# Kernel optimization log

Hardware: AMD Instinct MI355X
Metric: run time of the kernel (lower is better)

## Reference

```python
import jax, jax.numpy as jnp
import numpy as np

WIN = 7
DIM = 384
HEADS = 12
HEAD_DIM = DIM // HEADS


def relative_position_index(win):
    ch = np.arange(win)
    cw = np.arange(win)
    coords = np.stack(np.meshgrid(ch, cw, indexing='ij'))  # [2,w,w]
    cf = coords.reshape(2, -1)
    rel = cf[:, :, None] - cf[:, None, :]  # [2,ww,ww]
    rel = rel.transpose(1, 2, 0)
    rel[:, :, 0] += win - 1
    rel[:, :, 1] += win - 1
    rel[:, :, 0] *= 2 * win - 1
    return jnp.array(rel.sum(-1), dtype=jnp.int32)  # [ww,ww]


def setup_inputs() -> dict:
    key = jax.random.key(0)
    ks = jax.random.split(key, 9)
    B, S = 1024, WIN * WIN
    M = 16  # windows per image
    s = 1.0 / np.sqrt(DIM)
    return {
        'hidden_states': jax.random.normal(ks[0], (B, S, DIM), jnp.float32),
        'attention_mask': jax.random.normal(ks[1], (M, S, S), jnp.float32),
        'Wq': jax.random.normal(ks[2], (DIM, DIM), jnp.float32) * s,
        'bq': jnp.zeros((DIM,), jnp.float32),
        'Wk': jax.random.normal(ks[3], (DIM, DIM), jnp.float32) * s,
        'bk': jnp.zeros((DIM,), jnp.float32),
        'Wv': jax.random.normal(ks[4], (DIM, DIM), jnp.float32) * s,
        'bv': jnp.zeros((DIM,), jnp.float32),
        'rel_bias_table': jax.random.normal(ks[5], ((2 * WIN - 1) ** 2, HEADS), jnp.float32) * 0.02,
        'rel_index': relative_position_index(WIN),
    }


def reference(hidden_states, attention_mask, Wq, bq, Wk, bk, Wv, bv, rel_bias_table, rel_index):
    B, S, _ = hidden_states.shape
    q = (hidden_states @ Wq + bq).reshape(B, S, HEADS, HEAD_DIM)
    k = (hidden_states @ Wk + bk).reshape(B, S, HEADS, HEAD_DIM)
    v = (hidden_states @ Wv + bv).reshape(B, S, HEADS, HEAD_DIM)
    q = q / jnp.sqrt(jnp.float32(HEAD_DIM)).astype(q.dtype)
    attn = jnp.einsum('bqhd,bkhd->bhqk', q, k)  # [B,H,S,S]
    # relative position bias: gather + reshape + transpose -> [1,H,S,S]
    bias = rel_bias_table[rel_index.reshape(-1)].reshape(S, S, HEADS)
    attn = attn + jnp.transpose(bias, (2, 0, 1))[None]
    # shifted-window mask add: [B//M, M, H, S, S]
    Mw = attention_mask.shape[0]
    attn = attn.reshape(B // Mw, Mw, HEADS, S, S) + attention_mask[None, :, None, :, :]
    attn = attn.reshape(B, HEADS, S, S)
    attn = jax.nn.softmax(attn, axis=-1)
    out = jnp.einsum('bhqk,bkhd->bqhd', attn, v).reshape(B, S, DIM)
    return out
```

## Files before the change

### kernel.cpp

```cpp
#include <hip/hip_runtime.h>

typedef __attribute__((ext_vector_type(8))) short short8;
typedef __attribute__((ext_vector_type(4))) float f32x4;

__device__ __forceinline__ unsigned short f2bf(float f) {
  unsigned u = __builtin_bit_cast(unsigned, f);
  u += 0x7fffu + ((u >> 16) & 1u);
  return (unsigned short)(u >> 16);
}

__global__ __launch_bounds__(256) void k_prepw(const float* __restrict__ Wq, const float* __restrict__ Wk,
                                               const float* __restrict__ Wv, const float* __restrict__ bq,
                                               const float* __restrict__ bk, const float* __restrict__ bv,
                                               unsigned short* __restrict__ Wt, float* __restrict__ bvec) {
  int i = blockIdx.x * 256 + threadIdx.x;
  int n = i / 384, k = i - n * 384;
  int which = n / 384;
  int c = n - which * 384;
  const float* W = (which == 0) ? Wq : (which == 1) ? Wk : Wv;
  Wt[i] = f2bf(W[k * 384 + c]);
  if (k == 0) {
    const float* bb = (which == 0) ? bq : (which == 1) ? bk : bv;
    bvec[n] = bb[c];
  }
}

__global__ __launch_bounds__(256) void k_prept(const float* __restrict__ tab, const int* __restrict__ ridx,
                                               const float* __restrict__ am, float* __restrict__ T) {
  int i = blockIdx.x * 256 + threadIdx.x;
  int lane = i & 63;
  int rest = i >> 6;
  int ik = rest & 3, jq = (rest >> 2) & 3, wh = rest >> 4;
  int h = wh % 12, w = wh / 12;
  int lr = lane & 15, lg = lane >> 4;
  int q = jq * 16 + lr;
  f32x4 v;
  #pragma unroll
  for (int r = 0; r < 4; ++r) {
    int k = ik * 16 + lg * 4 + r;
    v[r] = (q < 49 && k < 49) ? tab[ridx[q * 49 + k] * 12 + h] + am[w * 2401 + q * 49 + k] : 0.f;
  }
  *(f32x4*)(T + (size_t)i * 4) = v;
}

__global__ __launch_bounds__(384, 3) void k_mega(const float* __restrict__ X,
                                                 const unsigned short* __restrict__ Wt,
                                                 const float* __restrict__ bvec,
                                                 const float* __restrict__ T,
                                                 float* __restrict__ out) {
  extern __shared__ unsigned short pool[];
  const int bid = blockIdx.x;
  const int w = bid >> 1, half = bid & 1;
  const int tid = threadIdx.x;
  const int lane = tid & 63, wid = tid >> 6;
  const int head = half * 6 + wid;
  const int lr = lane & 15, lg = lane >> 4;
  char* poolB = (char*)pool;

  #pragma unroll
  for (int it = 0; it < 8; ++it) {
    int c = tid + 384 * it;
    int row = c / 48, c8 = c - row * 48;
    short8 v = {0, 0, 0, 0, 0, 0, 0, 0};
    if (row < 49) {
      const float* p = X + ((size_t)(w * 49 + row)) * 384 + c8 * 8;
      f32x4 f0 = *(const f32x4*)p;
      f32x4 f1 = *(const f32x4*)(p + 4);
      v[0] = (short)f2bf(f0[0]); v[1] = (short)f2bf(f0[1]); v[2] = (short)f2bf(f0[2]); v[3] = (short)f2bf(f0[3]);
      v[4] = (short)f2bf(f1[0]); v[5] = (short)f2bf(f1[1]); v[6] = (short)f2bf(f1[2]); v[7] = (short)f2bf(f1[3]);
    }
    *(short8*)(poolB + row * 768 + ((c8 * 16) ^ ((row & 7) << 4))) = v;
  }
  __syncthreads();

  const unsigned swz = (unsigned)((lr & 7) << 4);
  unsigned hq[16], hk[16], hv[16];
  #pragma unroll
  for (int p = 0; p < 3; ++p) {
    const unsigned short* Bg = Wt + ((size_t)(p * 384 + head * 32 + lr)) * 384 + lg * 8;
    f32x4 acc[4][2] = {};
    short8 bB[4][2];
    #pragma unroll
    for (int k0 = 0; k0 < 3; ++k0) {
      bB[k0][0] = *(const short8*)(Bg + k0 * 32);
      bB[k0][1] = *(const short8*)(Bg + 16 * 384 + k0 * 32);
    }
    #pragma unroll
    for (int k = 0; k < 12; ++k) {
      if (k + 3 < 12) {
        bB[(k + 3) & 3][0] = *(const short8*)(Bg + (k + 3) * 32);
        bB[(k + 3) & 3][1] = *(const short8*)(Bg + 16 * 384 + (k + 3) * 32);
      }
      short8 aC[4];
      #pragma unroll
      for (int mi = 0; mi < 4; ++mi)
        aC[mi] = *(const short8*)(poolB + (16 * mi + lr) * 768 + (unsigned)((k * 64 + lg * 16) ^ swz));
      __builtin_amdgcn_s_setprio(1);
      #pragma unroll
      for (int mi = 0; mi < 4; ++mi)
        #pragma unroll
        for (int ni = 0; ni < 2; ++ni)
          acc[mi][ni] = __builtin_amdgcn_mfma_f32_16x16x32_bf16(aC[mi], bB[k & 3][ni], acc[mi][ni], 0, 0, 0);
      __builtin_amdgcn_s_setprio(0);
    }
    float scl = (p == 0) ? 0.17677669529663687f : 1.0f;
    unsigned* hd = (p == 0) ? hq : (p == 1) ? hk : hv;
    float b0 = bvec[p * 384 + head * 32 + lr];
    float b1 = bvec[p * 384 + head * 32 + 16 + lr];
    #pragma unroll
    for (int mi = 0; mi < 4; ++mi)
      #pragma unroll
      for (int ni = 0; ni < 2; ++ni) {
        float bb = ni ? b1 : b0;
        float v0 = (acc[mi][ni][0] + bb) * scl;
        float v1 = (acc[mi][ni][1] + bb) * scl;
        float v2 = (acc[mi][ni][2] + bb) * scl;
        float v3 = (acc[mi][ni][3] + bb) * scl;
        hd[(mi * 2 + ni) * 2 + 0] = (unsigned)f2bf(v0) | ((unsigned)f2bf(v1) << 16);
        hd[(mi * 2 + ni) * 2 + 1] = (unsigned)f2bf(v2) | ((unsigned)f2bf(v3) << 16);
      }
  }
  __syncthreads();

  unsigned short* reg = pool + wid * 6400;
  unsigned short* Qs = reg;
  unsigned short* Ks = reg + 1984;
  unsigned short* Vt = reg + 4096;
  char* Pb = (char*)reg;
  #pragma unroll
  for (int mi = 0; mi < 4; ++mi)
    #pragma unroll
    for (int ni = 0; ni < 2; ++ni) {
      int d = ni * 16 + lr;
      #pragma unroll
      for (int e = 0; e < 2; ++e) {
        int s0 = 16 * mi + 4 * lg + 2 * e;
        *(unsigned*)&Vt[d * 72 + s0] = hv[(mi * 2 + ni) * 2 + e];
      }
      #pragma unroll
      for (int r = 0; r < 4; ++r) {
        int s = 16 * mi + 4 * lg + r;
        if (s < 49) {
          unsigned short qv = (unsigned short)(hq[(mi * 2 + ni) * 2 + (r >> 1)] >> ((r & 1) * 16));
          unsigned short kv = (unsigned short)(hk[(mi * 2 + ni) * 2 + (r >> 1)] >> ((r & 1) * 16));
          Qs[s * 40 + d] = qv;
          Ks[s * 40 + d] = kv;
        }
      }
    }

  short8 qf[4], kf[4];
  #pragma unroll
  for (int t = 0; t < 4; ++t) {
    int rq = t * 16 + lr; if (rq > 48) rq = 48;
    qf[t] = *(const short8*)&Qs[rq * 40 + lg * 8];
    kf[t] = *(const short8*)&Ks[rq * 40 + lg * 8];
  }
  f32x4 sc[4][4] = {};
  #pragma unroll
  for (int ik = 0; ik < 4; ++ik)
    #pragma unroll
    for (int jq = 0; jq < 4; ++jq)
      sc[ik][jq] = __builtin_amdgcn_mfma_f32_16x16x32_bf16(kf[ik], qf[jq], sc[ik][jq], 0, 0, 0);

  const float* Tb = T + ((size_t)((w & 15) * 12 + head)) * 4096;
  #pragma unroll
  for (int jq = 0; jq < 4; ++jq) {
    #pragma unroll
    for (int ik = 0; ik < 4; ++ik) {
      f32x4 tv = *(const f32x4*)(Tb + ((jq * 4 + ik) * 64 + lane) * 4);
      #pragma unroll
      for (int r = 0; r < 4; ++r) {
        float v = sc[ik][jq][r] + tv[r];
        if (ik == 3) {
          if (r == 0) v = (lg == 0) ? v : -1e30f;
          else v = -1e30f;
        }
        sc[ik][jq][r] = v;
      }
    }
    float m = -1e30f;
    #pragma unroll
    for (int ik = 0; ik < 4; ++ik)
      #pragma unroll
      for (int r = 0; r < 4; ++r) m = fmaxf(m, sc[ik][jq][r]);
    m = fmaxf(m, __shfl_xor(m, 16));
    m = fmaxf(m, __shfl_xor(m, 32));
    float s = 0.f;
    #pragma unroll
    for (int ik = 0; ik < 4; ++ik)
      #pragma unroll
      for (int r = 0; r < 4; ++r) {
        float e = __expf(sc[ik][jq][r] - m);
        sc[ik][jq][r] = e;
        s += e;
      }
    s += __shfl_xor(s, 16);
    s += __shfl_xor(s, 32);
    float iv = 1.0f / s;
    int q = jq * 16 + lr;
    #pragma unroll
    for (int ik = 0; ik < 4; ++ik) {
      unsigned d0 = (unsigned)f2bf(sc[ik][jq][0] * iv) | ((unsigned)f2bf(sc[ik][jq][1] * iv) << 16);
      unsigned d1 = (unsigned)f2bf(sc[ik][jq][2] * iv) | ((unsigned)f2bf(sc[ik][jq][3] * iv) << 16);
      unsigned off = (unsigned)(q * 128 + ik * 32 + lg * 8) ^ ((unsigned)(lr & 7) << 4);
      *(uint2*)(Pb + off) = make_uint2(d0, d1);
    }
  }

  short8 vf[2][2];
  #pragma unroll
  for (int kk = 0; kk < 2; ++kk)
    #pragma unroll
    for (int nl = 0; nl < 2; ++nl)
      vf[kk][nl] = *(const short8*)&Vt[(nl * 16 + lr) * 72 + kk * 32 + lg * 8];
  f32x4 ao[4][2] = {};
  #pragma unroll
  for (int i = 0; i < 4; ++i) {
    short8 pf[2];
    #pragma unroll
    for (int kk = 0; kk < 2; ++kk) {
      unsigned off = (unsigned)((i * 16 + lr) * 128 + (kk * 4 + lg) * 16) ^ ((unsigned)(lr & 7) << 4);
      pf[kk] = *(const short8*)(Pb + off);
    }
    #pragma unroll
    for (int nl = 0; nl < 2; ++nl)
      #pragma unroll
      for (int kk = 0; kk < 2; ++kk)
        ao[i][nl] = __builtin_amdgcn_mfma_f32_16x16x32_bf16(pf[kk], vf[kk][nl], ao[i][nl], 0, 0, 0);
  }

  #pragma unroll
  for (int i = 0; i < 4; ++i) {
    #pragma unroll
    for (int j2 = 0; j2 < 4; ++j2) {
      int q = i * 16 + lg * 4 + j2;
      if (q < 49) {
        #pragma unroll
        for (int nl = 0; nl < 2; ++nl) {
          int d = nl * 16 + lr;
          out[((size_t)(w * 49 + q)) * 384 + head * 32 + d] = ao[i][nl][j2];
        }
      }
    }
  }
}

extern "C" void kernel_launch(void* const* d_in, const int* in_sizes, int n_in,
                              void* d_out, int out_size, void* d_ws, size_t ws_size,
                              hipStream_t stream) {
  const float* hs  = (const float*)d_in[0];
  const float* am  = (const float*)d_in[1];
  const float* Wq  = (const float*)d_in[2];
  const float* bq  = (const float*)d_in[3];
  const float* Wk  = (const float*)d_in[4];
  const float* bk  = (const float*)d_in[5];
  const float* Wv  = (const float*)d_in[6];
  const float* bv  = (const float*)d_in[7];
  const float* tab = (const float*)d_in[8];
  const int*   rix = (const int*)d_in[9];
  float* out = (float*)d_out;
  char* ws = (char*)d_ws;

  size_t o = 0;
  auto alloc = [&](size_t bytes) { size_t r = o; o = (o + bytes + 255) & ~(size_t)255; return r; };
  unsigned short* Wt   = (unsigned short*)(ws + alloc(1152ull * 384 * 2));
  float*          bvec = (float*)(ws + alloc(1152ull * 4));
  float*          Tt   = (float*)(ws + alloc(192ull * 4096 * 4));
  (void)ws_size; (void)in_sizes; (void)n_in; (void)out_size;

  hipFuncSetAttribute((const void*)k_mega, hipFuncAttributeMaxDynamicSharedMemorySize, 76800);

  k_prepw<<<1728, 256, 0, stream>>>(Wq, Wk, Wv, bq, bk, bv, Wt, bvec);
  k_prept<<<768, 256, 0, stream>>>(tab, rix, am, Tt);
  k_mega<<<2048, 384, 76800, stream>>>(hs, Wt, bvec, Tt, out);
}
```

Baseline: 318.5 us.

## Keep Q/K/P fragments in registers via transposed MFMA layouts, shrink LDS

The QKV projection now computes W^T·X^T, so the accumulator output lands directly in the fragment layout needed by 16x16x16 MFMAs for the scores and the PV product. This removes the LDS round trips for Q, K and P. Softmax normalisation is deferred to the output, which allows vectorized float4 stores. The V projection is moved after softmax, and LDS drops to 48KB, which could allow more blocks per CU. Block IDs are remapped to spread windows across XCDs. The cost is higher register pressure from holding the qfr, kfr and pfr fragments.

```diff
diff --git a/kernel.cpp b/kernel.cpp
--- a/kernel.cpp
+++ b/kernel.cpp
@@ -1,6 +1,7 @@
 #include <hip/hip_runtime.h>
 
 typedef __attribute__((ext_vector_type(8))) short short8;
+typedef __attribute__((ext_vector_type(4))) short s16x4;
 typedef __attribute__((ext_vector_type(4))) float f32x4;
 
 __device__ __forceinline__ unsigned short f2bf(float f) {
@@ -8,6 +9,16 @@
   u += 0x7fffu + ((u >> 16) & 1u);
   return (unsigned short)(u >> 16);
 }
+
+#if __has_builtin(__builtin_amdgcn_mfma_f32_16x16x16bf16_1k)
+#define MFMA16(A, B, C) __builtin_amdgcn_mfma_f32_16x16x16bf16_1k((A), (B), (C), 0, 0, 0)
+#else
+__device__ __forceinline__ f32x4 mfma16_asm(s16x4 a, s16x4 b, f32x4 c) {
+  asm volatile("v_mfma_f32_16x16x16_bf16 %0, %1, %2, %0" : "+v"(c) : "v"(a), "v"(b));
+  return c;
+}
+#define MFMA16(A, B, C) mfma16_asm((A), (B), (C))
+#endif
 
 __global__ __launch_bounds__(256) void k_prepw(const float* __restrict__ Wq, const float* __restrict__ Wk,
                                                const float* __restrict__ Wv, const float* __restrict__ bq,
@@ -49,13 +60,15 @@
                                                  const float* __restrict__ T,
                                                  float* __restrict__ out) {
   extern __shared__ unsigned short pool[];
-  const int bid = blockIdx.x;
+  int orig = blockIdx.x;
+  int bid = (orig & 7) * 256 + (orig >> 3);
   const int w = bid >> 1, half = bid & 1;
   const int tid = threadIdx.x;
   const int lane = tid & 63, wid = tid >> 6;
   const int head = half * 6 + wid;
   const int lr = lane & 15, lg = lane >> 4;
   char* poolB = (char*)pool;
+  const unsigned swz = (unsigned)((lr & 7) << 4);
 
   #pragma unroll
   for (int it = 0; it < 8; ++it) {
@@ -73,97 +86,62 @@
   }
   __syncthreads();
 
-  const unsigned swz = (unsigned)((lr & 7) << 4);
-  unsigned hq[16], hk[16], hv[16];
-  #pragma unroll
-  for (int p = 0; p < 3; ++p) {
-    const unsigned short* Bg = Wt + ((size_t)(p * 384 + head * 32 + lr)) * 384 + lg * 8;
-    f32x4 acc[4][2] = {};
-    short8 bB[4][2];
-    #pragma unroll
-    for (int k0 = 0; k0 < 3; ++k0) {
-      bB[k0][0] = *(const short8*)(Bg + k0 * 32);
-      bB[k0][1] = *(const short8*)(Bg + 16 * 384 + k0 * 32);
-    }
+  auto run_pass = [&](int p, float scl, s16x4 fr[2][4]) {
+    const unsigned short* Wg = Wt + ((size_t)(p * 384 + head * 32 + lr)) * 384 + lg * 8;
+    f32x4 acc[2][4] = {};
+    short8 wC[2], wN[2];
+    wC[0] = *(const short8*)(Wg);
+    wC[1] = *(const short8*)(Wg + 6144);
     #pragma unroll
     for (int k = 0; k < 12; ++k) {
-      if (k + 3 < 12) {
-        bB[(k + 3) & 3][0] = *(const short8*)(Bg + (k + 3) * 32);
-        bB[(k + 3) & 3][1] = *(const short8*)(Bg + 16 * 384 + (k + 3) * 32);
-      }
-      short8 aC[4];
-      #pragma unroll
-      for (int mi = 0; mi < 4; ++mi)
-        aC[mi] = *(const short8*)(poolB + (16 * mi + lr) * 768 + (unsigned)((k * 64 + lg * 16) ^ swz));
+      if (k < 11) {
+        wN[0] = *(const short8*)(Wg + (k + 1) * 32);
+        wN[1] = *(const short8*)(Wg + 6144 + (k + 1) * 32);
+      }
+      short8 xf[4];
+      #pragma unroll
+      for (int ni = 0; ni < 4; ++ni)
+        xf[ni] = *(const short8*)(poolB + (16 * ni + lr) * 768 + (unsigned)((k * 64 + lg * 16) ^ swz));
       __builtin_amdgcn_s_setprio(1);
       #pragma unroll
-      for (int mi = 0; mi < 4; ++mi)
+      for (int mi = 0; mi < 2; ++mi)
         #pragma unroll
-        for (int ni = 0; ni < 2; ++ni)
-          acc[mi][ni] = __builtin_amdgcn_mfma_f32_16x16x32_bf16(aC[mi], bB[k & 3][ni], acc[mi][ni], 0, 0, 0);
+        for (int ni = 0; ni < 4; ++ni)
+          acc[mi][ni] = __builtin_amdgcn_mfma_f32_16x16x32_bf16(wC[mi], xf[ni], acc[mi][ni], 0, 0, 0);
       __builtin_amdgcn_s_setprio(0);
-    }
-    float scl = (p == 0) ? 0.17677669529663687f : 1.0f;
-    unsigned* hd = (p == 0) ? hq : (p == 1) ? hk : hv;
-    float b0 = bvec[p * 384 + head * 32 + lr];
-    float b1 = bvec[p * 384 + head * 32 + 16 + lr];
-    #pragma unroll
-    for (int mi = 0; mi < 4; ++mi)
-      #pragma unroll
-      for (int ni = 0; ni < 2; ++ni) {
-        float bb = ni ? b1 : b0;
-        float v0 = (acc[mi][ni][0] + bb) * scl;
-        float v1 = (acc[mi][ni][1] + bb) * scl;
-        float v2 = (acc[mi][ni][2] + bb) * scl;
-        float v3 = (acc[mi][ni][3] + bb) * scl;
-        hd[(mi * 2 + ni) * 2 + 0] = (unsigned)f2bf(v0) | ((unsigned)f2bf(v1) << 16);
-        hd[(mi * 2 + ni) * 2 + 1] = (unsigned)f2bf(v2) | ((unsigned)f2bf(v3) << 16);
-      }
-  }
-  __syncthreads();
-
-  unsigned short* reg = pool + wid * 6400;
-  unsigned short* Qs = reg;
-  unsigned short* Ks = reg + 1984;
-  unsigned short* Vt = reg + 4096;
-  char* Pb = (char*)reg;
-  #pragma unroll
-  for (int mi = 0; mi < 4; ++mi)
-    #pragma unroll
-    for (int ni = 0; ni < 2; ++ni) {
-      int d = ni * 16 + lr;
-      #pragma unroll
-      for (int e = 0; e < 2; ++e) {
-        int s0 = 16 * mi + 4 * lg + 2 * e;
-        *(unsigned*)&Vt[d * 72 + s0] = hv[(mi * 2 + ni) * 2 + e];
-      }
-      #pragma unroll
-      for (int r = 0; r < 4; ++r) {
-        int s = 16 * mi + 4 * lg + r;
-        if (s < 49) {
-          unsigned short qv = (unsigned short)(hq[(mi * 2 + ni) * 2 + (r >> 1)] >> ((r & 1) * 16));
-          unsigned short kv = (unsigned short)(hk[(mi * 2 + ni) * 2 + (r >> 1)] >> ((r & 1) * 16));
-          Qs[s * 40 + d] = qv;
-          Ks[s * 40 + d] = kv;
-        }
-      }
-    }
-
-  short8 qf[4], kf[4];
-  #pragma unroll
-  for (int t = 0; t < 4; ++t) {
-    int rq = t * 16 + lr; if (rq > 48) rq = 48;
-    qf[t] = *(const short8*)&Qs[rq * 40 + lg * 8];
-    kf[t] = *(const short8*)&Ks[rq * 40 + lg * 8];
-  }
+      wC[0] = wN[0]; wC[1] = wN[1];
+    }
+    #pragma unroll
+    for (int mi = 0; mi < 2; ++mi) {
+      f32x4 bv = *(const f32x4*)(bvec + p * 384 + head * 32 + 16 * mi + 4 * lg);
+      #pragma unroll
+      for (int ni = 0; ni < 4; ++ni) {
+        s16x4 o;
+        #pragma unroll
+        for (int r = 0; r < 4; ++r) o[r] = (short)f2bf((acc[mi][ni][r] + bv[r]) * scl);
+        fr[mi][ni] = o;
+      }
+    }
+  };
+
+  s16x4 qfr[2][4], kfr[2][4];
+  run_pass(0, 0.17677669529663687f, qfr);
+  run_pass(1, 1.0f, kfr);
+
   f32x4 sc[4][4] = {};
-  #pragma unroll
-  for (int ik = 0; ik < 4; ++ik)
-    #pragma unroll
-    for (int jq = 0; jq < 4; ++jq)
-      sc[ik][jq] = __builtin_amdgcn_mfma_f32_16x16x32_bf16(kf[ik], qf[jq], sc[ik][jq], 0, 0, 0);
+  __builtin_amdgcn_s_setprio(1);
+  #pragma unroll
+  for (int dblk = 0; dblk < 2; ++dblk)
+    #pragma unroll
+    for (int ik = 0; ik < 4; ++ik)
+      #pragma unroll
+      for (int jq = 0; jq < 4; ++jq)
+        sc[ik][jq] = MFMA16(kfr[dblk][ik], qfr[dblk][jq], sc[ik][jq]);
+  __builtin_amdgcn_s_setprio(0);
 
   const float* Tb = T + ((size_t)((w & 15) * 12 + head)) * 4096;
+  s16x4 pfr[4][4];
+  float ivv[4];
   #pragma unroll
   for (int jq = 0; jq < 4; ++jq) {
     #pragma unroll
@@ -197,50 +175,56 @@
       }
     s += __shfl_xor(s, 16);
     s += __shfl_xor(s, 32);
-    float iv = 1.0f / s;
-    int q = jq * 16 + lr;
+    ivv[jq] = 1.0f / s;
     #pragma unroll
     for (int ik = 0; ik < 4; ++ik) {
-      unsigned d0 = (unsigned)f2bf(sc[ik][jq][0] * iv) | ((unsigned)f2bf(sc[ik][jq][1] * iv) << 16);
-      unsigned d1 = (unsigned)f2bf(sc[ik][jq][2] * iv) | ((unsigned)f2bf(sc[ik][jq][3] * iv) << 16);
-      unsigned off = (unsigned)(q * 128 + ik * 32 + lg * 8) ^ ((unsigned)(lr & 7) << 4);
-      *(uint2*)(Pb + off) = make_uint2(d0, d1);
-    }
-  }
-
-  short8 vf[2][2];
-  #pragma unroll
-  for (int kk = 0; kk < 2; ++kk)
-    #pragma unroll
-    for (int nl = 0; nl < 2; ++nl)
-      vf[kk][nl] = *(const short8*)&Vt[(nl * 16 + lr) * 72 + kk * 32 + lg * 8];
-  f32x4 ao[4][2] = {};
-  #pragma unroll
-  for (int i = 0; i < 4; ++i) {
-    short8 pf[2];
-    #pragma unroll
-    for (int kk = 0; kk < 2; ++kk) {
-      unsigned off = (unsigned)((i * 16 + lr) * 128 + (kk * 4 + lg) * 16) ^ ((unsigned)(lr & 7) << 4);
-      pf[kk] = *(const short8*)(Pb + off);
-    }
-    #pragma unroll
-    for (int nl = 0; nl < 2; ++nl)
-      #pragma unroll
-      for (int kk = 0; kk < 2; ++kk)
-        ao[i][nl] = __builtin_amdgcn_mfma_f32_16x16x32_bf16(pf[kk], vf[kk][nl], ao[i][nl], 0, 0, 0);
-  }
-
-  #pragma unroll
-  for (int i = 0; i < 4; ++i) {
-    #pragma unroll
-    for (int j2 = 0; j2 < 4; ++j2) {
-      int q = i * 16 + lg * 4 + j2;
-      if (q < 49) {
+      s16x4 o;
+      #pragma unroll
+      for (int r = 0; r < 4; ++r) o[r] = (short)f2bf(sc[ik][jq][r]);
+      pfr[ik][jq] = o;
+    }
+  }
+
+  s16x4 vfr[2][4];
+  run_pass(2, 1.0f, vfr);
+  __syncthreads();
+
+  unsigned short* Vt = pool + wid * 2304;
+  #pragma unroll
+  for (int mi = 0; mi < 2; ++mi)
+    #pragma unroll
+    for (int ni = 0; ni < 4; ++ni)
+      #pragma unroll
+      for (int r = 0; r < 4; ++r)
+        Vt[(16 * mi + 4 * lg + r) * 72 + 16 * ni + lr] = (unsigned short)vfr[mi][ni][r];
+
+  f32x4 ao[2][4] = {};
+  #pragma unroll
+  for (int st = 0; st < 4; ++st) {
+    s16x4 vread[2];
+    #pragma unroll
+    for (int dt = 0; dt < 2; ++dt)
+      vread[dt] = *(const s16x4*)&Vt[(16 * dt + lr) * 72 + 16 * st + 4 * lg];
+    __builtin_amdgcn_s_setprio(1);
+    #pragma unroll
+    for (int dt = 0; dt < 2; ++dt)
+      #pragma unroll
+      for (int jq = 0; jq < 4; ++jq)
+        ao[dt][jq] = MFMA16(vread[dt], pfr[st][jq], ao[dt][jq]);
+    __builtin_amdgcn_s_setprio(0);
+  }
+
+  #pragma unroll
+  for (int jq = 0; jq < 4; ++jq) {
+    int q = 16 * jq + lr;
+    if (q < 49) {
+      float iv = ivv[jq];
+      #pragma unroll
+      for (int dt = 0; dt < 2; ++dt) {
+        f32x4 o;
         #pragma unroll
-        for (int nl = 0; nl < 2; ++nl) {
-          int d = nl * 16 + lr;
-          out[((size_t)(w * 49 + q)) * 384 + head * 32 + d] = ao[i][nl][j2];
-        }
+        for (int r = 0; r < 4; ++r) o[r] = ao[dt][jq][r] * iv;
+        *(f32x4*)(out + ((size_t)(w * 49 + q)) * 384 + head * 32 + 16 * dt + 4 * lg) = o;
       }
     }
   }
@@ -269,9 +253,7 @@
   float*          Tt   = (float*)(ws + alloc(192ull * 4096 * 4));
   (void)ws_size; (void)in_sizes; (void)n_in; (void)out_size;
 
-  hipFuncSetAttribute((const void*)k_mega, hipFuncAttributeMaxDynamicSharedMemorySize, 76800);
-
   k_prepw<<<1728, 256, 0, stream>>>(Wq, Wk, Wv, bq, bk, bv, Wt, bvec);
   k_prept<<<768, 256, 0, stream>>>(tab, rix, am, Tt);
-  k_mega<<<2048, 384, 76800, stream>>>(hs, Wt, bvec, Tt, out);
-}
+  k_mega<<<2048, 384, 49152, stream>>>(hs, Wt, bvec, Tt, out);
+}
```

Result: faster. 300.4 us (-5.7%).
